# Kernel tuning notes

Measured on AMD Instinct MI355X. Metric: run time of the kernel, lower is better.

Reference implementation:

```python
import jax, jax.numpy as jnp
import numpy as np

DIM = 512
FEAT = 64
BATCH = 2048

def setup_inputs() -> dict:
    key = jax.random.key(0)
    kx, kw, kb = jax.random.split(key, 3)
    x = jax.random.normal(kx, (BATCH, DIM, FEAT), dtype=jnp.float32)
    # torch Linear weight is [out, in]; emulate Kaiming-uniform-ish init scale
    bound = 1.0 / np.sqrt(FEAT)
    W = jax.random.uniform(kw, (DIM, FEAT, FEAT), dtype=jnp.float32, minval=-bound, maxval=bound)
    b = jax.random.uniform(kb, (DIM, FEAT), dtype=jnp.float32, minval=-bound, maxval=bound)
    return {"x": x, "W": W, "b": b}

def reference(x, W, b):
    # per-slice Linear: out[:, d, :] = x[:, d, :] @ W[d].T + b[d]
    # fused as one batched contraction over the feature (input) axis 'f'
    return jnp.einsum('bdf,dgf->bdg', x, W) + b[None, :, :]
```

## Files before the change

### kernel.cpp

```cpp
#include <hip/hip_runtime.h>
#include <hip/hip_bf16.h>

#define DIM  512
#define FEAT 64
#define BATCH 2048

#define ROWS_PER_BLOCK 512
#define TILES_PER_WAVE 8
#define SLOTS 2

using bf16x8 = __attribute__((ext_vector_type(8))) short;
using f32x4  = __attribute__((ext_vector_type(4))) float;

typedef __attribute__((address_space(3))) float lds_f;
typedef __attribute__((address_space(1))) const float glb_f;

__device__ inline short f2bf(float f) {
    unsigned int u = __float_as_uint(f);
    u += 0x7fffu + ((u >> 16) & 1u);
    return (short)(u >> 16);
}

__device__ inline bf16x8 cvt8(float4 a, float4 b) {
    bf16x8 r;
    r[0] = f2bf(a.x); r[1] = f2bf(a.y); r[2] = f2bf(a.z); r[3] = f2bf(a.w);
    r[4] = f2bf(b.x); r[5] = f2bf(b.y); r[6] = f2bf(b.z); r[7] = f2bf(b.w);
    return r;
}

__global__ __launch_bounds__(256, 4)
void split_linear_kernel(const float* __restrict__ x,
                         const float* __restrict__ W,
                         const float* __restrict__ bias,
                         float* __restrict__ out)
{
    __shared__ float xlds[4][SLOTS][1024];
    __shared__ float obuf[4][1024];
    __shared__ float blds[FEAT];

    const int id    = blockIdx.x;
    const int xcd   = id & 7;
    const int chunk = id >> 3;
    const int nid   = xcd * 256 + chunk;
    const int d     = nid & (DIM - 1);
    const int b0    = (nid >> 9) * ROWS_PER_BLOCK;

    const int tid  = threadIdx.x;
    const int wave = tid >> 6;
    const int lane = tid & 63;
    const int lr   = lane & 15;
    const int lk   = lane >> 4;

    if (tid < FEAT) blds[tid] = bias[(size_t)d * FEAT + tid];
    __syncthreads();

    bf16x8 wf[2][4];
#pragma unroll
    for (int mt = 0; mt < 4; ++mt) {
        const float* wrow = W + ((size_t)d * FEAT + mt * 16 + lr) * FEAT + lk * 8;
#pragma unroll
        for (int ks = 0; ks < 2; ++ks) {
            float4 w0 = *(const float4*)(wrow + ks * 32);
            float4 w1 = *(const float4*)(wrow + ks * 32 + 4);
            wf[ks][mt] = cvt8(w0, w1);
        }
    }

    auto stage = [&](int slot, int tt) {
#pragma unroll
        for (int i = 0; i < 4; ++i) {
            const int r = i * 4 + (lane >> 4);
            const int c = (lane & 15) ^ (r & 7);
            const float* gp = x + ((size_t)(b0 + tt * 16 + r) * DIM + d) * FEAT + c * 4;
            __builtin_amdgcn_global_load_lds((glb_f*)gp,
                                             (lds_f*)&xlds[wave][slot][i * 256],
                                             16, 0, 0);
        }
    };

    stage(0, wave);
    stage(1, 4 + wave);

#pragma unroll
    for (int t = 0; t < TILES_PER_WAVE; ++t) {
        if (t == 0)                asm volatile("s_waitcnt vmcnt(4)"  ::: "memory");
        else if (t == 1 || t == 7) asm volatile("s_waitcnt vmcnt(8)"  ::: "memory");
        else                       asm volatile("s_waitcnt vmcnt(12)" ::: "memory");
        __builtin_amdgcn_sched_barrier(0);

        const float* sl = &xlds[wave][t & 1][0];
        float4 p0a = *(const float4*)&sl[lr * 64 + (((lk * 2 + 0) ^ (lr & 7)) << 2)];
        float4 p0b = *(const float4*)&sl[lr * 64 + (((lk * 2 + 1) ^ (lr & 7)) << 2)];
        float4 p1a = *(const float4*)&sl[lr * 64 + (((8 + lk * 2 + 0) ^ (lr & 7)) << 2)];
        float4 p1b = *(const float4*)&sl[lr * 64 + (((8 + lk * 2 + 1) ^ (lr & 7)) << 2)];

        bf16x8 af0 = cvt8(p0a, p0b);
        bf16x8 af1 = cvt8(p1a, p1b);
        __builtin_amdgcn_sched_barrier(0);

        if (t + 2 < TILES_PER_WAVE)
            stage(t & 1, (t + 2) * 4 + wave);

        f32x4 acc[4];
#pragma unroll
        for (int mt = 0; mt < 4; ++mt)
            acc[mt] = *(const f32x4*)&blds[mt * 16 + lk * 4];
#pragma unroll
        for (int mt = 0; mt < 4; ++mt)
            acc[mt] = __builtin_amdgcn_mfma_f32_16x16x32_bf16(wf[0][mt], af0, acc[mt], 0, 0, 0);
#pragma unroll
        for (int mt = 0; mt < 4; ++mt)
            acc[mt] = __builtin_amdgcn_mfma_f32_16x16x32_bf16(wf[1][mt], af1, acc[mt], 0, 0, 0);

#pragma unroll
        for (int mt = 0; mt < 4; ++mt) {
            const int c  = mt * 4 + lk;
            const int pc = (c & 8) | ((c & 7) ^ (lr & 7));
            *(f32x4*)&obuf[wave][lr * 64 + pc * 4] = acc[mt];
        }

        const int orow0 = b0 + (t * 4 + wave) * 16;
#pragma unroll
        for (int j = 0; j < 4; ++j) {
            const int rr  = j * 4 + (lane >> 4);
            const int cc  = lane & 15;
            const int pc2 = (cc & 8) | ((cc & 7) ^ (rr & 7));
            f32x4 v = *(const f32x4*)&obuf[wave][rr * 64 + pc2 * 4];
            __builtin_nontemporal_store(v,
                (f32x4*)(out + ((size_t)(orow0 + rr) * DIM + d) * FEAT + cc * 4));
        }
        __builtin_amdgcn_sched_barrier(0);
    }
}

extern "C" void kernel_launch(void* const* d_in, const int* in_sizes, int n_in,
                              void* d_out, int out_size, void* d_ws, size_t ws_size,
                              hipStream_t stream) {
    const float* x    = (const float*)d_in[0];
    const float* W    = (const float*)d_in[1];
    const float* bias = (const float*)d_in[2];
    float* out        = (float*)d_out;

    dim3 grid(DIM * (BATCH / ROWS_PER_BLOCK), 1, 1);
    dim3 block(256, 1, 1);
    split_linear_kernel<<<grid, block, 0, stream>>>(x, W, bias, out);
}
```

Before: 106.0 us.

## Reuse input LDS slot for output staging and keep bias in registers

Removes the separate output staging buffer and bias LDS array. Results are written back into the x tile's LDS slot, and the bias is held in registers loaded from global memory. This cuts LDS per block so occupancy can rise to 5 blocks per CU, with launch bounds updated to match. In exchange, the prefetch of tile t+2 must wait until the slot's outputs have been read back, which shortens how far ahead loads are issued and lowers the vmcnt wait thresholds.

Result: slower. 188.2 us (+77.5%).

```diff
diff --git a/kernel.cpp b/kernel.cpp
--- a/kernel.cpp
+++ b/kernel.cpp
@@ -7,7 +7,6 @@
 
 #define ROWS_PER_BLOCK 512
 #define TILES_PER_WAVE 8
-#define SLOTS 2
 
 using bf16x8 = __attribute__((ext_vector_type(8))) short;
 using f32x4  = __attribute__((ext_vector_type(4))) float;
@@ -28,15 +27,13 @@
     return r;
 }
 
-__global__ __launch_bounds__(256, 4)
+__global__ __launch_bounds__(256, 5)
 void split_linear_kernel(const float* __restrict__ x,
                          const float* __restrict__ W,
                          const float* __restrict__ bias,
                          float* __restrict__ out)
 {
-    __shared__ float xlds[4][SLOTS][1024];
-    __shared__ float obuf[4][1024];
-    __shared__ float blds[FEAT];
+    __shared__ float xlds[4][2][1024];
 
     const int id    = blockIdx.x;
     const int xcd   = id & 7;
@@ -51,9 +48,6 @@
     const int lr   = lane & 15;
     const int lk   = lane >> 4;
 
-    if (tid < FEAT) blds[tid] = bias[(size_t)d * FEAT + tid];
-    __syncthreads();
-
     bf16x8 wf[2][4];
 #pragma unroll
     for (int mt = 0; mt < 4; ++mt) {
@@ -65,6 +59,11 @@
             wf[ks][mt] = cvt8(w0, w1);
         }
     }
+
+    f32x4 bias4[4];
+#pragma unroll
+    for (int mt = 0; mt < 4; ++mt)
+        bias4[mt] = *(const f32x4*)(bias + (size_t)d * FEAT + mt * 16 + lk * 4);
 
     auto stage = [&](int slot, int tt) {
 #pragma unroll
@@ -83,12 +82,14 @@
 
 #pragma unroll
     for (int t = 0; t < TILES_PER_WAVE; ++t) {
-        if (t == 0)                asm volatile("s_waitcnt vmcnt(4)"  ::: "memory");
-        else if (t == 1 || t == 7) asm volatile("s_waitcnt vmcnt(8)"  ::: "memory");
-        else                       asm volatile("s_waitcnt vmcnt(12)" ::: "memory");
+        const int s = t & 1;
+        if (t == 0 || t == TILES_PER_WAVE - 1)
+            asm volatile("s_waitcnt vmcnt(4)" ::: "memory");
+        else
+            asm volatile("s_waitcnt vmcnt(8)" ::: "memory");
         __builtin_amdgcn_sched_barrier(0);
 
-        const float* sl = &xlds[wave][t & 1][0];
+        float* sl = &xlds[wave][s][0];
         float4 p0a = *(const float4*)&sl[lr * 64 + (((lk * 2 + 0) ^ (lr & 7)) << 2)];
         float4 p0b = *(const float4*)&sl[lr * 64 + (((lk * 2 + 1) ^ (lr & 7)) << 2)];
         float4 p1a = *(const float4*)&sl[lr * 64 + (((8 + lk * 2 + 0) ^ (lr & 7)) << 2)];
@@ -96,15 +97,10 @@
 
         bf16x8 af0 = cvt8(p0a, p0b);
         bf16x8 af1 = cvt8(p1a, p1b);
-        __builtin_amdgcn_sched_barrier(0);
-
-        if (t + 2 < TILES_PER_WAVE)
-            stage(t & 1, (t + 2) * 4 + wave);
 
         f32x4 acc[4];
 #pragma unroll
-        for (int mt = 0; mt < 4; ++mt)
-            acc[mt] = *(const f32x4*)&blds[mt * 16 + lk * 4];
+        for (int mt = 0; mt < 4; ++mt) acc[mt] = bias4[mt];
 #pragma unroll
         for (int mt = 0; mt < 4; ++mt)
             acc[mt] = __builtin_amdgcn_mfma_f32_16x16x32_bf16(wf[0][mt], af0, acc[mt], 0, 0, 0);
@@ -115,8 +111,8 @@
 #pragma unroll
         for (int mt = 0; mt < 4; ++mt) {
             const int c  = mt * 4 + lk;
-            const int pc = (c & 8) | ((c & 7) ^ (lr & 7));
-            *(f32x4*)&obuf[wave][lr * 64 + pc * 4] = acc[mt];
+            const int pc = c ^ (lr & 7);
+            *(f32x4*)&sl[lr * 64 + pc * 4] = acc[mt];
         }
 
         const int orow0 = b0 + (t * 4 + wave) * 16;
@@ -124,12 +120,15 @@
         for (int j = 0; j < 4; ++j) {
             const int rr  = j * 4 + (lane >> 4);
             const int cc  = lane & 15;
-            const int pc2 = (cc & 8) | ((cc & 7) ^ (rr & 7));
-            f32x4 v = *(const f32x4*)&obuf[wave][rr * 64 + pc2 * 4];
+            const int pc2 = cc ^ (rr & 7);
+            f32x4 v = *(const f32x4*)&sl[rr * 64 + pc2 * 4];
             __builtin_nontemporal_store(v,
                 (f32x4*)(out + ((size_t)(orow0 + rr) * DIM + d) * FEAT + cc * 4));
         }
         __builtin_amdgcn_sched_barrier(0);
+
+        if (t + 2 < TILES_PER_WAVE)
+            stage(s, (t + 2) * 4 + wave);
     }
 }
 
```
